# Kernel tuning notes

Hardware: AMD Instinct MI355X
Metric: run time of the kernel (lower is better)

## Reference

```python
import jax, jax.numpy as jnp
import numpy as np

K = 3          # kernel_size
S = 2          # stride
NEW = 2        # new_size = int(ratio * stride)
C = 32         # channels
BN_EPS = 1e-5


def _unfold(x, oh, ow):
    # torch.nn.Unfold(K, dilation=1, padding=(K-1)//2, stride=S) reshaped to
    # [B, C, K, K, oh, ow] (channel slowest, then kernel rows, kernel cols).
    p = (K - 1) // 2
    xp = jnp.pad(x, ((0, 0), (0, 0), (p, p), (p, p)))
    rows = []
    for i in range(K):
        cols = []
        for j in range(K):
            cols.append(xp[:, :, i:i + S * (oh - 1) + 1:S, j:j + S * (ow - 1) + 1:S])
        rows.append(jnp.stack(cols, axis=2))          # [B,C,K,oh,ow]
    return jnp.stack(rows, axis=2)                    # [B,C,K,K,oh,ow]


def reference(x, conv_w, bn_gamma, bn_beta, bn_mean, bn_var):
    B, _, W, H = x.shape
    oh = -(-W // S)
    ow = -(-H // S)
    patches = _unfold(x, oh, ow)                      # [B,C,K,K,oh,ow]

    # three max reductions over different unfolded axes
    x1 = patches.max(axis=1).reshape(B, K * K, oh, ow)    # over channels
    x2 = patches.max(axis=2).reshape(B, C * K, oh, ow)    # over kernel rows
    x3 = patches.max(axis=3).reshape(B, C * K, oh, ow)    # over kernel cols
    feat = jnp.concatenate([x1, x2, x3], axis=1)          # [B, K*K+2*C*K, oh, ow]

    # ConvModule: 1x1 conv (no bias, since BN) -> BN (eval stats) -> ReLU
    y = jnp.einsum('bihw,oi->bohw', feat, conv_w)
    inv = (bn_gamma / jnp.sqrt(bn_var + BN_EPS))[None, :, None, None]
    y = (y - bn_mean[None, :, None, None]) * inv + bn_beta[None, :, None, None]
    y = jax.nn.relu(y)

    # dynamic kernel: [B, C, K*K, NEW, NEW, oh, ow]
    w = y.reshape(B, C, K * K, NEW, NEW, oh, ow)
    px = patches.reshape(B, C, K * K, 1, 1, oh, ow)
    out = jnp.mean(px * w, axis=2)                    # [B,C,NEW,NEW,oh,ow]
    out = out.transpose(0, 1, 4, 2, 5, 3)             # [B,C,oh,NEW,ow,NEW]
    out = out.reshape(B, C, oh * NEW, ow * NEW)
    return out[:, :, :W, :H]


def setup_inputs() -> dict:
    key = jax.random.key(0)
    k1, k2 = jax.random.split(key)
    B, W, H = 8, 128, 128
    in_ch = K * C * 2 + K * K                         # 201
    out_ch = C * NEW * NEW * K * K                    # 1152
    x = jax.random.normal(k1, (B, C, W, H), dtype=jnp.float32)
    conv_w = jax.random.normal(k2, (out_ch, in_ch), dtype=jnp.float32) * 0.02
    return {
        'x': x,
        'conv_w': conv_w,
        'bn_gamma': jnp.ones((out_ch,), jnp.float32),
        'bn_beta': jnp.zeros((out_ch,), jnp.float32),
        'bn_mean': jnp.zeros((out_ch,), jnp.float32),
        'bn_var': jnp.ones((out_ch,), jnp.float32),
    }
```

## Files before the change

kernel.cpp:

```cpp
#include <hip/hip_runtime.h>
#include <math.h>

typedef __bf16 v8bf __attribute__((ext_vector_type(8)));
typedef float  v4f  __attribute__((ext_vector_type(4)));

constexpr int Bsz  = 8;
constexpr int Cch  = 32;
constexpr int WIMG = 128;
constexpr int OH   = 64;
constexpr int OW   = 64;
constexpr int INCH = 201;
constexpr int KP   = 224;
constexpr int NK   = 7;
constexpr int OUTCH = 1152;
constexpr int MTOT = Bsz * OH * OW;
constexpr float BN_EPS = 1e-5f;

constexpr size_t WT_BYTES = (size_t)NK * OUTCH * 32 * 2;
constexpr size_t BIAS_OFF = WT_BYTES;
constexpr size_t FEAT_OFF = BIAS_OFF + OUTCH * 4;

typedef const void __attribute__((address_space(1)))* gas_ptr;
typedef void __attribute__((address_space(3)))* las_ptr;
__device__ __forceinline__ void load16_lds(const void* g, void* l) {
    __builtin_amdgcn_global_load_lds((gas_ptr)(uintptr_t)g, (las_ptr)(uintptr_t)l, 16, 0, 0);
}

constexpr int SXS = 132;
constexpr int FEAT_BLOCKS = Bsz * OH;
constexpr int NPREP = OUTCH * KP + OUTCH;
constexpr int PREP_BLOCKS = (NPREP + 255) / 256;

__global__ __launch_bounds__(256)
void prep_feat_kernel(const float* __restrict__ x,
                      const float* __restrict__ conv_w,
                      const float* __restrict__ gamma,
                      const float* __restrict__ beta,
                      const float* __restrict__ mean,
                      const float* __restrict__ var,
                      __bf16* __restrict__ Wt,
                      float* __restrict__ biasp,
                      __bf16* __restrict__ feat) {
    __shared__ __align__(16) float sx[Cch * 3 * SXS];
    __shared__ __align__(16) float cmax[3 * SXS];
    __shared__ __align__(16) __bf16 sfeat[NK * OW * 32];

    const int t = threadIdx.x;

    if (blockIdx.x >= FEAT_BLOCKS) {
        int idx = ((int)blockIdx.x - FEAT_BLOCKS) * 256 + t;
        const int nW = OUTCH * KP;
        if (idx < nW) {
            int o = idx / KP;
            int f = idx - o * KP;
            float inv = gamma[o] * rsqrtf(var[o] + BN_EPS);
            float v = (f < INCH) ? conv_w[o * INCH + f] * inv : 0.0f;
            Wt[((size_t)(f >> 5) * OUTCH + o) * 32 + (f & 31)] = (__bf16)v;
        } else if (idx < nW + OUTCH) {
            int o = idx - nW;
            float inv = gamma[o] * rsqrtf(var[o] + BN_EPS);
            biasp[o] = beta[o] - mean[o] * inv;
        }
        return;
    }

    const int b  = blockIdx.x >> 6;
    const int ho = blockIdx.x & 63;

    for (int idx = t; idx < Cch * 3 * 32; idx += 256) {
        int c   = idx / 96;
        int rem = idx - c * 96;
        int i   = rem >> 5;
        int q   = rem & 31;
        int r   = 2 * ho - 1 + i;
        float4 v = make_float4(0.f, 0.f, 0.f, 0.f);
        if (r >= 0 && r < WIMG)
            v = *(const float4*)(x + (((size_t)(b * Cch + c) * WIMG) + r) * WIMG + q * 4);
        float* dst = sx + (c * 3 + i) * SXS + q * 4 + 1;
        dst[0] = v.x; dst[1] = v.y; dst[2] = v.z; dst[3] = v.w;
    }
    if (t < 96) {
        float* row = sx + t * SXS;
        row[0] = 0.0f; row[129] = 0.0f; row[130] = 0.0f; row[131] = 0.0f;
    }
    __syncthreads();

    if (t < 99) {
        int i = t / 33, cg = t - i * 33;
        const float4* base = (const float4*)sx + i * (SXS / 4) + cg;
        float4 m = base[0];
        #pragma unroll 4
        for (int c = 1; c < Cch; ++c) {
            float4 v = base[(size_t)c * (3 * SXS / 4)];
            m.x = fmaxf(m.x, v.x); m.y = fmaxf(m.y, v.y);
            m.z = fmaxf(m.z, v.z); m.w = fmaxf(m.w, v.w);
        }
        ((float4*)cmax)[i * (SXS / 4) + cg] = m;
    }
    __syncthreads();

    for (int idx = t; idx < 9 * 64; idx += 256) {
        int f = idx >> 6, wo = idx & 63;
        int i = f / 3, j = f - 3 * i;
        sfeat[wo * 32 + f] = (__bf16)cmax[i * SXS + 2 * wo + j];
    }
    {
        const int wp = t & 31, g = t >> 5;
        const int wo0 = 2 * wp;
        #pragma unroll
        for (int cl = 0; cl < 4; ++cl) {
            int c = g * 4 + cl;
            float v[3][5];
            #pragma unroll
            for (int i = 0; i < 3; ++i) {
                const float* row = sx + (c * 3 + i) * SXS + 4 * wp;
                float4 q = *(const float4*)row;
                v[i][0] = q.x; v[i][1] = q.y; v[i][2] = q.z; v[i][3] = q.w;
                v[i][4] = row[4];
            }
            #pragma unroll
            for (int i = 0; i < 3; ++i) {
                int f = 105 + c * 3 + i;
                float a0 = fmaxf(fmaxf(v[i][0], v[i][1]), v[i][2]);
                float a1 = fmaxf(fmaxf(v[i][2], v[i][3]), v[i][4]);
                sfeat[(f >> 5) * 2048 + wo0 * 32 + (f & 31)]       = (__bf16)a0;
                sfeat[(f >> 5) * 2048 + (wo0 + 1) * 32 + (f & 31)] = (__bf16)a1;
            }
            #pragma unroll
            for (int j = 0; j < 3; ++j) {
                int f = 9 + c * 3 + j;
                float a0 = fmaxf(fmaxf(v[0][j], v[1][j]), v[2][j]);
                float a1 = fmaxf(fmaxf(v[0][j + 2], v[1][j + 2]), v[2][j + 2]);
                sfeat[(f >> 5) * 2048 + wo0 * 32 + (f & 31)]       = (__bf16)a0;
                sfeat[(f >> 5) * 2048 + (wo0 + 1) * 32 + (f & 31)] = (__bf16)a1;
            }
        }
    }
    for (int idx = t; idx < 64 * 23; idx += 256) {
        int wo = idx / 23, fo = idx - wo * 23;
        int f = 201 + fo;
        sfeat[6 * 2048 + wo * 32 + (f & 31)] = (__bf16)0.0f;
    }
    __syncthreads();

    const size_t spat0 = (size_t)(b * OH + ho) * OW;
    #pragma unroll
    for (int kc = 0; kc < NK; ++kc) {
        float4 vv = ((const float4*)sfeat)[kc * 256 + t];
        ((float4*)((char*)feat + ((size_t)kc * MTOT + spat0) * 64))[t] = vv;
    }
}

constexpr int YS  = 148;
constexpr int REG = 16 * YS;
__global__ __launch_bounds__(256, 2)
void gemm_kernel(const __bf16* __restrict__ feat,
                 const __bf16* __restrict__ Wt,
                 const float* __restrict__ biasp,
                 const float* __restrict__ x,
                 float* __restrict__ out) {
    __shared__ __align__(16) unsigned char lds[37888];

    const int t    = threadIdx.x;
    const int nb   = (int)blockIdx.x >> 8;
    const int mb   = (int)blockIdx.x & 255;
    const int M0   = mb * 128;
    const int N0   = nb * 144;
    const int wave = t >> 6, lane = t & 63, quad = lane >> 4, l16 = lane & 15;

    auto issue = [&](int ks, int buf) {
        const char* Ag = (const char*)feat + ((size_t)ks * MTOT + M0) * 64;
        char* Ab = (char*)lds + buf * 8192;
        #pragma unroll
        for (int i = 0; i < 2; ++i) {
            int off = (wave * 2 + i) * 1024 + lane * 16;
            load16_lds(Ag + off, Ab + off);
        }
        const char* Bg = (const char*)Wt + ((size_t)ks * OUTCH + N0) * 64;
        char* Bb = (char*)lds + 16384 + buf * 9216;
        #pragma unroll
        for (int i = 0; i < 2; ++i) {
            int off = (wave * 2 + i) * 1024 + lane * 16;
            load16_lds(Bg + off, Bb + off);
        }
        if (wave == 0) {
            int off2 = 8192 + lane * 16;
            load16_lds(Bg + off2, Bb + off2);
        }
    };

    v4f acc[2][9];
    #pragma unroll
    for (int mt = 0; mt < 2; ++mt)
        #pragma unroll
        for (int nt = 0; nt < 9; ++nt)
            acc[mt][nt] = (v4f){0.f, 0.f, 0.f, 0.f};

    issue(0, 0);
    __syncthreads();

    for (int ks = 0; ks < NK; ++ks) {
        const int cur = ks & 1;
        if (ks + 1 < NK) issue(ks + 1, cur ^ 1);

        const char* Ab = (const char*)lds + cur * 8192;
        const char* Bb = (const char*)lds + 16384 + cur * 9216;
        v8bf af[2];
        #pragma unroll
        for (int mt = 0; mt < 2; ++mt)
            af[mt] = *(const v8bf*)(Ab + (wave * 32 + mt * 16 + l16) * 64 + quad * 16);
        #pragma unroll
        for (int nt = 0; nt < 9; ++nt) {
            v8bf bf = *(const v8bf*)(Bb + (nt * 16 + l16) * 64 + quad * 16);
            #pragma unroll
            for (int mt = 0; mt < 2; ++mt)
                acc[mt][nt] = __builtin_amdgcn_mfma_f32_16x16x32_bf16(
                    af[mt], bf, acc[mt][nt], 0, 0, 0);
        }
        __syncthreads();
    }

    float bia[9];
    #pragma unroll
    for (int nt = 0; nt < 9; ++nt) bia[nt] = biasp[N0 + nt * 16 + l16];

    float* yw = (float*)lds + wave * REG;
    const int cl  = lane >> 4;
    const int wl  = lane & 15;
    const int cg  = nb * 4 + cl;
    const float s9 = 1.0f / 9.0f;

    #pragma unroll
    for (int p = 0; p < 2; ++p) {
        #pragma unroll
        for (int nt = 0; nt < 9; ++nt)
            #pragma unroll
            for (int r = 0; r < 4; ++r)
                yw[(quad * 4 + r) * YS + nt * 16 + l16] =
                    fmaxf(acc[p][nt][r] + bia[nt], 0.0f);

        const int mg  = M0 + wave * 32 + p * 16 + wl;
        const int bb  = mg >> 12;
        const int hob = (mg >> 6) & 63;
        const int wo  = mg & 63;
        const float* xc = x + (size_t)(bb * Cch + cg) * WIMG * WIMG;

        float pt[9];
        #pragma unroll
        for (int qi = 0; qi < 3; ++qi) {
            int r = 2 * hob - 1 + qi;
            #pragma unroll
            for (int qj = 0; qj < 3; ++qj) {
                int col = 2 * wo - 1 + qj;
                float v = 0.0f;
                if (r >= 0 && r < WIMG && col >= 0 && col < WIMG)
                    v = xc[r * WIMG + col];
                pt[qi * 3 + qj] = v;
            }
        }
        const float4* yrow = (const float4*)(yw + wl * YS + cl * 36);
        float o00 = 0.f, o01 = 0.f, o10 = 0.f, o11 = 0.f;
        #pragma unroll
        for (int q = 0; q < 9; ++q) {
            float4 yv = yrow[q];
            float pq = pt[q];
            o00 = fmaf(pq, yv.x, o00);
            o01 = fmaf(pq, yv.y, o01);
            o10 = fmaf(pq, yv.z, o10);
            o11 = fmaf(pq, yv.w, o11);
        }
        size_t obase = (((size_t)(bb * Cch + cg) * WIMG) + 2 * hob) * WIMG + 2 * wo;
        *(float2*)(out + obase)        = make_float2(o00 * s9, o01 * s9);
        *(float2*)(out + obase + WIMG) = make_float2(o10 * s9, o11 * s9);
    }
}

extern "C" void kernel_launch(void* const* d_in, const int* in_sizes, int n_in,
                              void* d_out, int out_size, void* d_ws, size_t ws_size,
                              hipStream_t stream) {
    const float* x      = (const float*)d_in[0];
    const float* conv_w = (const float*)d_in[1];
    const float* gamma  = (const float*)d_in[2];
    const float* beta   = (const float*)d_in[3];
    const float* mean   = (const float*)d_in[4];
    const float* var    = (const float*)d_in[5];
    float* out = (float*)d_out;

    __bf16* Wt    = (__bf16*)d_ws;
    float*  biasp = (float*)((char*)d_ws + BIAS_OFF);
    __bf16* feat  = (__bf16*)((char*)d_ws + FEAT_OFF);

    prep_feat_kernel<<<FEAT_BLOCKS + PREP_BLOCKS, 256, 0, stream>>>(
        x, conv_w, gamma, beta, mean, var, Wt, biasp, feat);
    gemm_kernel<<<(OUTCH / 144) * (MTOT / 128), 256, 0, stream>>>(feat, Wt, biasp, x, out);
}
```

Measured before the change: 118.6 us.

## Load GEMM A fragments directly into registers and repad epilogue LDS rows

The A operand (features) of the GEMM is now loaded straight from global memory into register fragments, with a one-step register prefetch, instead of being staged through LDS. Only the weight tile B is still double-buffered in LDS. The epilogue row stride changes from 148 to 150 floats, and the y reads drop from float4 to float2 so they stay aligned, aiming to reduce LDS bank conflicts. The cost is more registers and uncoalesced 16-byte global loads for A, plus the total LDS allocation grows slightly.

```diff
diff --git a/kernel.cpp b/kernel.cpp
--- a/kernel.cpp
+++ b/kernel.cpp
@@ -151,7 +151,7 @@
     }
 }
 
-constexpr int YS  = 148;
+constexpr int YS  = 150;
 constexpr int REG = 16 * YS;
 __global__ __launch_bounds__(256, 2)
 void gemm_kernel(const __bf16* __restrict__ feat,
@@ -159,7 +159,7 @@
                  const float* __restrict__ biasp,
                  const float* __restrict__ x,
                  float* __restrict__ out) {
-    __shared__ __align__(16) unsigned char lds[37888];
+    __shared__ __align__(16) unsigned char lds[38400];
 
     const int t    = threadIdx.x;
     const int nb   = (int)blockIdx.x >> 8;
@@ -168,16 +168,9 @@
     const int N0   = nb * 144;
     const int wave = t >> 6, lane = t & 63, quad = lane >> 4, l16 = lane & 15;
 
-    auto issue = [&](int ks, int buf) {
-        const char* Ag = (const char*)feat + ((size_t)ks * MTOT + M0) * 64;
-        char* Ab = (char*)lds + buf * 8192;
-        #pragma unroll
-        for (int i = 0; i < 2; ++i) {
-            int off = (wave * 2 + i) * 1024 + lane * 16;
-            load16_lds(Ag + off, Ab + off);
-        }
+    auto issueB = [&](int ks, int buf) {
         const char* Bg = (const char*)Wt + ((size_t)ks * OUTCH + N0) * 64;
-        char* Bb = (char*)lds + 16384 + buf * 9216;
+        char* Bb = (char*)lds + buf * 9216;
         #pragma unroll
         for (int i = 0; i < 2; ++i) {
             int off = (wave * 2 + i) * 1024 + lane * 16;
@@ -188,6 +181,12 @@
             load16_lds(Bg + off2, Bb + off2);
         }
     };
+    auto loadA = [&](int ks, v8bf af[2]) {
+        const char* Ag = (const char*)feat +
+            ((size_t)ks * MTOT + M0 + wave * 32 + l16) * 64 + quad * 16;
+        af[0] = *(const v8bf*)(Ag);
+        af[1] = *(const v8bf*)(Ag + 16 * 64);
+    };
 
     v4f acc[2][9];
     #pragma unroll
@@ -196,28 +195,30 @@
         for (int nt = 0; nt < 9; ++nt)
             acc[mt][nt] = (v4f){0.f, 0.f, 0.f, 0.f};
 
-    issue(0, 0);
+    v8bf afc[2], afn[2];
+    loadA(0, afc);
+    issueB(0, 0);
     __syncthreads();
 
     for (int ks = 0; ks < NK; ++ks) {
         const int cur = ks & 1;
-        if (ks + 1 < NK) issue(ks + 1, cur ^ 1);
-
-        const char* Ab = (const char*)lds + cur * 8192;
-        const char* Bb = (const char*)lds + 16384 + cur * 9216;
-        v8bf af[2];
-        #pragma unroll
-        for (int mt = 0; mt < 2; ++mt)
-            af[mt] = *(const v8bf*)(Ab + (wave * 32 + mt * 16 + l16) * 64 + quad * 16);
+        if (ks + 1 < NK) {
+            issueB(ks + 1, cur ^ 1);
+            loadA(ks + 1, afn);
+        }
+
+        const char* Bb = (const char*)lds + cur * 9216;
         #pragma unroll
         for (int nt = 0; nt < 9; ++nt) {
             v8bf bf = *(const v8bf*)(Bb + (nt * 16 + l16) * 64 + quad * 16);
             #pragma unroll
             for (int mt = 0; mt < 2; ++mt)
                 acc[mt][nt] = __builtin_amdgcn_mfma_f32_16x16x32_bf16(
-                    af[mt], bf, acc[mt][nt], 0, 0, 0);
+                    afc[mt], bf, acc[mt][nt], 0, 0, 0);
         }
         __syncthreads();
+        afc[0] = afn[0];
+        afc[1] = afn[1];
     }
 
     float bia[9];
@@ -258,16 +259,17 @@
                 pt[qi * 3 + qj] = v;
             }
         }
-        const float4* yrow = (const float4*)(yw + wl * YS + cl * 36);
+        const float2* yrow = (const float2*)(yw + wl * YS + cl * 36);
         float o00 = 0.f, o01 = 0.f, o10 = 0.f, o11 = 0.f;
         #pragma unroll
         for (int q = 0; q < 9; ++q) {
-            float4 yv = yrow[q];
+            float2 y0 = yrow[2 * q];
+            float2 y1 = yrow[2 * q + 1];
             float pq = pt[q];
-            o00 = fmaf(pq, yv.x, o00);
-            o01 = fmaf(pq, yv.y, o01);
-            o10 = fmaf(pq, yv.z, o10);
-            o11 = fmaf(pq, yv.w, o11);
+            o00 = fmaf(pq, y0.x, o00);
+            o01 = fmaf(pq, y0.y, o01);
+            o10 = fmaf(pq, y1.x, o10);
+            o11 = fmaf(pq, y1.y, o11);
         }
         size_t obase = (((size_t)(bb * Cch + cg) * WIMG) + 2 * hob) * WIMG + 2 * wo;
         *(float2*)(out + obase)        = make_float2(o00 * s9, o01 * s9);
```

Result: no change. 118.8 us (+0.2%).
